# Optimization experiments

Hardware: AMD Instinct MI355X
Metric: run time of the kernel (lower is better)

The kernel has to match this reference:

```python
import jax, jax.numpy as jnp
import numpy as np


def setup_inputs() -> dict:
    key = jax.random.key(0)
    x = jax.random.normal(key, (8, 2048, 3), dtype=jnp.float32)
    return {"x": x, "k": 16}


def reference(x, k):
    b, n, d = x.shape
    xf = x.reshape(b * n, d)                      # flatten across batch, as in the torch module
    sq = jnp.sum(xf * xf, axis=1, keepdims=True)  # [BN, 1]
    pair = 2.0 * (xf @ xf.T) - sq - sq.T          # [BN, BN] = -dist^2
    # torch topk(largest=False) on pair == largest of (-pair) == largest squared distance
    neg_vals, idx = jax.lax.top_k(-pair, k + 1)   # [BN, k+1]
    dists = -neg_vals
    dists = dists[:, 1:].reshape(b, n, k)
    idx = idx[:, 1:].reshape(b, n, k)
    return dists, idx
```

## Files before the change

### kernel.cpp

```cpp
#include <hip/hip_runtime.h>
#include <stdint.h>

#define BN       16384
#define NTILES   256
#define NB       64
#define NW       16
#define KOUT     16
#define MARGIN   0.01f
#define PPT      16

typedef float v2f __attribute__((ext_vector_type(2)));
union F4 { float4 f4; v2f p[2]; float f[4]; };

#define WS_TAB    0
#define WS_IDX    (WS_TAB + BN * 16)
#define WS_BND    (WS_IDX + BN * 4)

__device__ __forceinline__ unsigned key_u(unsigned u) {
    return u ^ ((unsigned)((int)u >> 31) | 0x80000000u);
}
__device__ __forceinline__ unsigned wshr1(unsigned v, unsigned oldv) {
    return (unsigned)__builtin_amdgcn_update_dpp((int)oldv, (int)v, 0x138 ,
                                                 0xF, 0xF, false);
}
#define RL16(T) __uint_as_float((unsigned)__builtin_amdgcn_readlane(__float_as_int(T), 16))

__device__ __forceinline__ float sq_of(float gx, float gy, float gz) {
    return __fadd_rn(__fadd_rn(__fmul_rn(gx, gx), __fmul_rn(gy, gy)), __fmul_rn(gz, gz));
}
__device__ __forceinline__ int bucket_of(float sq) {
    const float rho = __fsqrt_rn(sq);
    int b = (int)(64.0f * (1.0f - rho * 0.2f));
    return (b < 0) ? 0 : ((b > 63) ? 63 : b);
}

#define DRAIN(m, p, jvec, T, J)                                                     \
    while (m) {                                                                     \
        const int b_ = (int)__builtin_ctzll(m);                                     \
        m &= m - 1;                                                                 \
        const float pc_ = __uint_as_float(                                          \
            (unsigned)__builtin_amdgcn_readlane(__float_as_int(p), b_));            \
        const unsigned jc_ = (unsigned)__builtin_amdgcn_readlane((int)(jvec), b_);  \
        const float Tup_ =                                                          \
            __uint_as_float(wshr1(__float_as_uint(T), 0xFF800000u ));       \
        const unsigned Jup_ = wshr1((J), 0u);                                       \
        const bool lt_ = (pc_ < Tup_) || ((pc_ == Tup_) && (jc_ < Jup_));           \
        const float Tn_ = lt_ ? Tup_ : pc_;                                         \
        const unsigned Jn_ = lt_ ? Jup_ : jc_;                                      \
        const bool sel_ = (pc_ < (T)) || ((pc_ == (T)) && (jc_ < (J)));             \
        (T) = sel_ ? Tn_ : (T);                                                     \
        (J) = sel_ ? Jn_ : (J);                                                     \
    }

#define EVALC(c, d2)                                                                \
    asm("v_pk_mul_f32 %0, %1, %2 op_sel:[0,0] op_sel_hi:[0,1]"                      \
        : "=v"(d2) : "v"((c).p[0]), "v"(c0A));                                      \
    asm("v_pk_fma_f32 %0, %1, %2, %0 op_sel:[1,0,0] op_sel_hi:[1,1,1]"              \
        : "+v"(d2) : "v"((c).p[0]), "v"(c1A));                                      \
    asm("v_pk_fma_f32 %0, %1, %2, %0 op_sel:[0,0,0] op_sel_hi:[0,1,1]"              \
        : "+v"(d2) : "v"((c).p[1]), "v"(c2A));                                      \
    asm("v_pk_add_f32 %0, %0, %1" : "+v"(d2) : "v"(nsq01));                         \
    asm("v_pk_add_f32 %0, %0, %1 op_sel:[0,1] op_sel_hi:[1,1]"                      \
        : "+v"(d2) : "v"((c).p[1]));

#define TILE_AT(t)                                                                  \
    F4 c; c.f4 = tab[(t) * 64 + lane];                                              \
    const unsigned jvec = idxarr[(t) * 64 + lane];                                  \
    v2f d2; EVALC(c, d2)

#define PROCESS_LOADED()                                                            \
    do {                                                                            \
        uint64_t m0 = __ballot(d2[0] <= fF0);                                       \
        uint64_t m1 = __ballot(d2[1] <= fF1);                                       \
        if (m0 | m1) {                                                              \
            const float p0 = d2[0], p1 = d2[1];                                     \
            DRAIN(m0, p0, jvec, T0, J0)                                             \
            DRAIN(m1, p1, jvec, T1, J1)                                             \
            fF0 = RL16(T0); thr0 = __fsub_rn(-fF0, MARGIN);                         \
            fF1 = RL16(T1); thr1 = __fsub_rn(-fF1, MARGIN);                         \
        }                                                                           \
    } while (0)

__device__ __forceinline__ void presort64(float p, unsigned j, int lane, double* sw,
                                          float& T, unsigned& J) {
    const double dm = (double)key_u(__float_as_uint(p)) * 16384.0 + (double)j;
    sw[lane] = dm;
    unsigned rank = 0;
    const char* sb = (const char*)sw;
    unsigned off = (unsigned)lane * 8u;
#pragma unroll 7
    for (int s = 1; s < 64; ++s) {
        off = (off + 8u) & 511u;
        const double dn = *(const double*)(sb + off);
        rank += (dn < dm) ? 1u : 0u;
    }
    sw[rank] = __longlong_as_double(
        (long long)(((unsigned long long)j << 32) | __float_as_uint(p)));
    const unsigned long long v = (unsigned long long)__double_as_longlong(sw[lane]);
    T = __uint_as_float((unsigned)(v & 0xFFFFFFFFull));
    J = (unsigned)(v >> 32);
}

__global__ __launch_bounds__(1024) void k_prep(const float* __restrict__ x,
                                               float4* __restrict__ tab,
                                               unsigned* __restrict__ idxarr,
                                               float2* __restrict__ bnd) {
    __shared__ unsigned cnt[NW * 65];
    __shared__ unsigned base[NB];
    __shared__ unsigned tmaxs[NTILES];
    const int tid  = threadIdx.x;
    const int wid  = tid >> 6;
    for (int i = tid; i < NW * 65; i += 1024) cnt[i] = 0u;
    if (tid < NTILES) tmaxs[tid] = 0u;
    __syncthreads();

    float px[PPT], py[PPT], pz[PPT], psq[PPT];
    int pb[PPT];
#pragma unroll
    for (int k = 0; k < PPT; ++k) {
        const int i = tid + k * 1024;
        const float gx = x[3 * i], gy = x[3 * i + 1], gz = x[3 * i + 2];
        const float sq = sq_of(gx, gy, gz);
        px[k] = gx; py[k] = gy; pz[k] = gz; psq[k] = sq;
        pb[k] = bucket_of(sq);
        atomicAdd(&cnt[wid * 65 + pb[k]], 1u);
    }
    __syncthreads();
    if (tid < NB) {
        unsigned s = 0;
#pragma unroll
        for (int w = 0; w < NW; ++w) s += cnt[w * 65 + tid];
        base[tid] = s;
    }
    __syncthreads();
    if (tid == 0) {
        unsigned s = 0;
        for (int b = 0; b < NB; ++b) { const unsigned t = base[b]; base[b] = s; s += t; }
    }
    __syncthreads();
    if (tid < NB) {
        unsigned s = base[tid];
#pragma unroll
        for (int w = 0; w < NW; ++w) {
            const unsigned t = cnt[w * 65 + tid];
            cnt[w * 65 + tid] = s;
            s += t;
        }
    }
    __syncthreads();
#pragma unroll
    for (int k = 0; k < PPT; ++k) {
        const int i = tid + k * 1024;
        const unsigned pos = atomicAdd(&cnt[wid * 65 + pb[k]], 1u);
        tab[pos] = make_float4(px[k], py[k], pz[k], -psq[k]);
        idxarr[pos] = (unsigned)i;
        atomicMax(&tmaxs[pos >> 6], __float_as_uint(psq[k]));
    }
    __syncthreads();
    for (int s = 1; s < NTILES; s <<= 1) {
        unsigned v = 0;
        if (tid < NTILES) {
            v = tmaxs[tid];
            if (tid + s < NTILES) { const unsigned w = tmaxs[tid + s]; v = (w > v) ? w : v; }
        }
        __syncthreads();
        if (tid < NTILES) tmaxs[tid] = v;
        __syncthreads();
    }
    if (tid < NTILES) {
        const float B = __uint_as_float(tmaxs[tid]);
        const float sqB_up = __uint_as_float(__float_as_uint(__fsqrt_rn(B)) + 2u);
        bnd[tid] = make_float2(B, sqB_up);
    }
}

__global__ __launch_bounds__(256) void knn_far_kernel(
    const float* __restrict__ x, const float4* __restrict__ tab,
    const unsigned* __restrict__ idxarr, const float2* __restrict__ bnd,
    float* __restrict__ out_d, float* __restrict__ out_i) {
    __shared__ double swall[4 * 64];
    const int tid  = threadIdx.x;
    const int lane = tid & 63;
    const int wid  = tid >> 6;
    double* sw = swall + wid * 64;
    const int q0 = (blockIdx.x * 4 + wid) * 2;
    const int q1 = q0 + 1;

    const float a0 = x[3 * q0], a1 = x[3 * q0 + 1], a2 = x[3 * q0 + 2];
    const float b0 = x[3 * q1], b1 = x[3 * q1 + 1], b2 = x[3 * q1 + 2];
    const float sq0 = sq_of(a0, a1, a2), sq1 = sq_of(b0, b1, b2);
    const v2f nsq01 = {-sq0, -sq1};
    const v2f c0A = {2.0f * a0, 2.0f * b0};
    const v2f c1A = {2.0f * a1, 2.0f * b1};
    const v2f c2A = {2.0f * a2, 2.0f * b2};
    const float twor0 = 2.0f * __uint_as_float(__float_as_uint(__fsqrt_rn(sq0)) + 2u);
    const float twor1 = 2.0f * __uint_as_float(__float_as_uint(__fsqrt_rn(sq1)) + 2u);

    float T0, T1; unsigned J0, J1;
    float fF0, fF1, thr0, thr1;

    {
        TILE_AT(0)
        presort64(d2[0], jvec, lane, sw, T0, J0);
        presort64(d2[1], jvec, lane, sw, T1, J1);
        fF0 = RL16(T0); thr0 = __fsub_rn(-fF0, MARGIN);
        fF1 = RL16(T1); thr1 = __fsub_rn(-fF1, MARGIN);
    }
#pragma unroll
    for (int t = 1; t < 4; ++t) {
        TILE_AT(t)
        PROCESS_LOADED();
    }
    for (int t = 4; t < NTILES; ++t) {
        const float2 bd = bnd[t];
        const float u0 = __builtin_fmaf(twor0, bd.y, __fadd_rn(sq0, bd.x));
        const float u1 = __builtin_fmaf(twor1, bd.y, __fadd_rn(sq1, bd.x));
        if (u0 < thr0 && u1 < thr1) break;
        TILE_AT(t)
        PROCESS_LOADED();
    }

    if (lane >= 1 && lane <= KOUT) {
        const int r = lane - 1;
        out_d[q0 * KOUT + r] = T0;
        out_i[q0 * KOUT + r] = (float)J0;
        out_d[q1 * KOUT + r] = T1;
        out_i[q1 * KOUT + r] = (float)J1;
    }
}

extern "C" void kernel_launch(void* const* d_in, const int* in_sizes, int n_in,
                              void* d_out, int out_size, void* d_ws, size_t ws_size,
                              hipStream_t stream) {
    const float* x = (const float*)d_in[0];
    char* ws = (char*)d_ws;
    float4*   tab    = (float4*)(ws + WS_TAB);
    unsigned* idxarr = (unsigned*)(ws + WS_IDX);
    float2*   bnd    = (float2*)(ws + WS_BND);
    float* out_d = (float*)d_out;
    float* out_i = out_d + (size_t)BN * KOUT;

    hipLaunchKernelGGL(k_prep, dim3(1), dim3(1024), 0, stream, x, tab, idxarr, bnd);
    hipLaunchKernelGGL(knn_far_kernel, dim3(BN / 8), dim3(256), 0, stream,
                       x, tab, idxarr, bnd, out_d, out_i);
}
```

Baseline: 90.98 us.

## Replace LDS rank presort with ballot bisection and prefetch next tile in far loop

The shared-memory rank-based presort of the first tile is replaced by a 32-step ballot/popcount bisection on ordered float keys. This finds the 17th-smallest key as the initial threshold, and the candidates below it are inserted through the existing DRAIN path. The main tile loop is software-pipelined so the next tile's table, index and bound loads are issued before the current tile is evaluated, hiding global load latency. The change removes LDS use and the 63-step double compare loop, at the cost of extra registers and a possibly wasted prefetch when the loop exits early.

After: 102.6 us. 1.13x slower.

```diff
diff --git a/kernel.cpp b/kernel.cpp
--- a/kernel.cpp
+++ b/kernel.cpp
@@ -18,6 +18,9 @@
 
 __device__ __forceinline__ unsigned key_u(unsigned u) {
     return u ^ ((unsigned)((int)u >> 31) | 0x80000000u);
+}
+__device__ __forceinline__ unsigned key2f_u(unsigned t) {
+    return t ^ ((unsigned)((int)(~t) >> 31) | 0x80000000u);
 }
 __device__ __forceinline__ unsigned wshr1(unsigned v, unsigned oldv) {
     return (unsigned)__builtin_amdgcn_update_dpp((int)oldv, (int)v, 0x138 ,
@@ -81,26 +84,6 @@
         }                                                                           \
     } while (0)
 
-__device__ __forceinline__ void presort64(float p, unsigned j, int lane, double* sw,
-                                          float& T, unsigned& J) {
-    const double dm = (double)key_u(__float_as_uint(p)) * 16384.0 + (double)j;
-    sw[lane] = dm;
-    unsigned rank = 0;
-    const char* sb = (const char*)sw;
-    unsigned off = (unsigned)lane * 8u;
-#pragma unroll 7
-    for (int s = 1; s < 64; ++s) {
-        off = (off + 8u) & 511u;
-        const double dn = *(const double*)(sb + off);
-        rank += (dn < dm) ? 1u : 0u;
-    }
-    sw[rank] = __longlong_as_double(
-        (long long)(((unsigned long long)j << 32) | __float_as_uint(p)));
-    const unsigned long long v = (unsigned long long)__double_as_longlong(sw[lane]);
-    T = __uint_as_float((unsigned)(v & 0xFFFFFFFFull));
-    J = (unsigned)(v >> 32);
-}
-
 __global__ __launch_bounds__(1024) void k_prep(const float* __restrict__ x,
                                                float4* __restrict__ tab,
                                                unsigned* __restrict__ idxarr,
@@ -178,11 +161,9 @@
     const float* __restrict__ x, const float4* __restrict__ tab,
     const unsigned* __restrict__ idxarr, const float2* __restrict__ bnd,
     float* __restrict__ out_d, float* __restrict__ out_i) {
-    __shared__ double swall[4 * 64];
     const int tid  = threadIdx.x;
     const int lane = tid & 63;
     const int wid  = tid >> 6;
-    double* sw = swall + wid * 64;
     const int q0 = (blockIdx.x * 4 + wid) * 2;
     const int q1 = q0 + 1;
 
@@ -196,28 +177,65 @@
     const float twor0 = 2.0f * __uint_as_float(__float_as_uint(__fsqrt_rn(sq0)) + 2u);
     const float twor1 = 2.0f * __uint_as_float(__float_as_uint(__fsqrt_rn(sq1)) + 2u);
 
-    float T0, T1; unsigned J0, J1;
+    float T0 = __uint_as_float(0x7F800000u), T1 = T0;
+    unsigned J0 = 0u, J1 = 0u;
     float fF0, fF1, thr0, thr1;
 
     {
-        TILE_AT(0)
-        presort64(d2[0], jvec, lane, sw, T0, J0);
-        presort64(d2[1], jvec, lane, sw, T1, J1);
-        fF0 = RL16(T0); thr0 = __fsub_rn(-fF0, MARGIN);
-        fF1 = RL16(T1); thr1 = __fsub_rn(-fF1, MARGIN);
+        F4 c; c.f4 = tab[lane];
+        const unsigned jvec = idxarr[lane];
+        v2f d2; EVALC(c, d2)
+        const unsigned kk0 = key_u(__float_as_uint(d2[0]));
+        const unsigned kk1 = key_u(__float_as_uint(d2[1]));
+        unsigned lo0 = 0u, hi0 = 0xFFFFFFFFu;
+        unsigned lo1 = 0u, hi1 = 0xFFFFFFFFu;
+        for (int it = 0; it < 32; ++it) {
+            const unsigned mid0 = lo0 + ((hi0 - lo0) >> 1);
+            const unsigned mid1 = lo1 + ((hi1 - lo1) >> 1);
+            const int n0 = __popcll(__ballot(kk0 <= mid0));
+            const int n1 = __popcll(__ballot(kk1 <= mid1));
+            if (n0 >= KOUT + 1) hi0 = mid0; else lo0 = mid0 + 1u;
+            if (n1 >= KOUT + 1) hi1 = mid1; else lo1 = mid1 + 1u;
+        }
+        fF0 = __uint_as_float(key2f_u(lo0)); thr0 = __fsub_rn(-fF0, MARGIN);
+        fF1 = __uint_as_float(key2f_u(lo1)); thr1 = __fsub_rn(-fF1, MARGIN);
+        uint64_t m0 = __ballot(kk0 <= lo0);
+        uint64_t m1 = __ballot(kk1 <= lo1);
+        const float p0 = d2[0], p1 = d2[1];
+        DRAIN(m0, p0, jvec, T0, J0)
+        DRAIN(m1, p1, jvec, T1, J1)
     }
 #pragma unroll
     for (int t = 1; t < 4; ++t) {
         TILE_AT(t)
         PROCESS_LOADED();
     }
+
+    F4 cp; cp.f4 = tab[4 * 64 + lane];
+    unsigned jp = idxarr[4 * 64 + lane];
+    float2 bdp = bnd[4];
     for (int t = 4; t < NTILES; ++t) {
-        const float2 bd = bnd[t];
-        const float u0 = __builtin_fmaf(twor0, bd.y, __fadd_rn(sq0, bd.x));
-        const float u1 = __builtin_fmaf(twor1, bd.y, __fadd_rn(sq1, bd.x));
+        const float u0 = __builtin_fmaf(twor0, bdp.y, __fadd_rn(sq0, bdp.x));
+        const float u1 = __builtin_fmaf(twor1, bdp.y, __fadd_rn(sq1, bdp.x));
         if (u0 < thr0 && u1 < thr1) break;
-        TILE_AT(t)
-        PROCESS_LOADED();
+        const int tn = (t + 1 < NTILES) ? (t + 1) : t;
+        F4 c2; c2.f4 = tab[tn * 64 + lane];
+        const unsigned j2 = idxarr[tn * 64 + lane];
+        const float2 bd2 = bnd[tn];
+        {
+            v2f d2; EVALC(cp, d2)
+            uint64_t m0 = __ballot(d2[0] <= fF0);
+            uint64_t m1 = __ballot(d2[1] <= fF1);
+            if (m0 | m1) {
+                const float p0 = d2[0], p1 = d2[1];
+                const unsigned jvv = jp;
+                DRAIN(m0, p0, jvv, T0, J0)
+                DRAIN(m1, p1, jvv, T1, J1)
+                fF0 = RL16(T0); thr0 = __fsub_rn(-fF0, MARGIN);
+                fF1 = RL16(T1); thr1 = __fsub_rn(-fF1, MARGIN);
+            }
+        }
+        cp = c2; jp = j2; bdp = bd2;
     }
 
     if (lane >= 1 && lane <= KOUT) {
```
